# Kernel tuning notes

Measured on AMD Instinct MI355X. Metric: run time of the kernel, lower is better.

The kernel has to match this reference:

```python
import jax, jax.numpy as jnp
import numpy as np

N = 100000   # nodes
E = 3200000  # random edges (before self-loops)
D = 20       # hidden width


def setup_inputs() -> dict:
    key = jax.random.key(0)
    k = jax.random.split(key, 8)
    return {
        "feat": jax.random.normal(k[0], (N, 1), jnp.float32),
        "W_start": jax.random.normal(k[1], (1, D), jnp.float32) * 0.5,
        "b_start": jnp.zeros((D,), jnp.float32),
        "W_mid": jax.random.normal(k[2], (18, D, D), jnp.float32) * (1.0 / np.sqrt(D)),
        "b_mid": jnp.zeros((18, D), jnp.float32),
        "W_final": jax.random.normal(k[3], (D, D), jnp.float32) * (1.0 / np.sqrt(D)),
        "b_final": jnp.zeros((D,), jnp.float32),
        "src": jax.random.randint(k[4], (E,), 0, N, jnp.int32),
        "dst": jax.random.randint(k[5], (E,), 0, N, jnp.int32),
    }


def reference(feat, W_start, b_start, W_mid, b_mid, W_final, b_final, src, dst):
    # dgl.add_self_loop
    loop = jnp.arange(N, dtype=src.dtype)
    src2 = jnp.concatenate([src, loop])
    dst2 = jnp.concatenate([dst, loop])

    ones = jnp.ones(src2.shape[0], jnp.float32)
    out_deg = jax.ops.segment_sum(ones, src2, num_segments=N)
    in_deg = jax.ops.segment_sum(ones, dst2, num_segments=N)
    # with self-loops degrees >= 1; clamp defensively like DGL
    dout = jnp.power(jnp.maximum(out_deg, 1.0), -0.5)  # [N]
    din = jnp.power(jnp.maximum(in_deg, 1.0), -0.5)    # [N]

    def conv(h, W, b):
        # GraphConv norm='both': D_out^{-1/2} on source, sum-aggregate, D_in^{-1/2} on dest
        hw = (h * dout[:, None]) @ W                   # [N, out]
        agg = jax.ops.segment_sum(hw[src2], dst2, num_segments=N)
        return agg * din[:, None] + b

    h = jax.nn.relu(conv(feat, W_start, b_start))

    def step(h, wb):
        W, b = wb
        return jax.nn.relu(conv(h, W, b)), None

    h, _ = jax.lax.scan(step, h, (W_mid, b_mid))
    h = conv(h, W_final, b_final)
    return h[None]  # unsqueeze(0) -> [1, N, D]
```

## Files before the change

kernel.cpp:

```cpp
#include <hip/hip_runtime.h>

#define DH   20
#define BKS  10
#define BKN  1024
#define MAXK 128
#define CHUNK 8192


__global__ void zero_bhist2(int* __restrict__ bhist_d, int* __restrict__ bhist_s) {
    int i = threadIdx.x;
    if (i < MAXK) { bhist_d[i] = 0; bhist_s[i] = 0; }
}

__global__ __launch_bounds__(256) void bucket_hist2(const int* __restrict__ src,
        const int* __restrict__ dst, int* __restrict__ bhist_d,
        int* __restrict__ bhist_s, int E, int K) {
    __shared__ int hd[MAXK];
    __shared__ int hs[MAXK];
    for (int i = threadIdx.x; i < K; i += blockDim.x) { hd[i] = 0; hs[i] = 0; }
    __syncthreads();
    int lo = blockIdx.x * CHUNK;
    int hi = lo + CHUNK; if (hi > E) hi = E;
    for (int e = lo + (int)threadIdx.x; e < hi; e += 256) {
        atomicAdd(&hd[__builtin_nontemporal_load(&dst[e]) >> BKS], 1);
        atomicAdd(&hs[__builtin_nontemporal_load(&src[e]) >> BKS], 1);
    }
    __syncthreads();
    for (int i = threadIdx.x; i < K; i += blockDim.x) {
        if (hd[i]) atomicAdd(&bhist_d[i], hd[i]);
        if (hs[i]) atomicAdd(&bhist_s[i], hs[i]);
    }
}

__global__ void bucket_scan2(const int* __restrict__ bhist_d, int* __restrict__ bbase_d,
                             int* __restrict__ bcursor_d, const int* __restrict__ bhist_s,
                             int* __restrict__ bbase_s, int* __restrict__ bcursor_s, int K) {
    if (threadIdx.x == 0) {
        int run = 0;
        for (int k = 0; k < K; ++k) {
            bbase_d[k] = run; bcursor_d[k] = run;
            run += bhist_d[k];
        }
        bbase_d[K] = run;
    } else if (threadIdx.x == 1) {
        int run = 0;
        for (int k = 0; k < K; ++k) {
            bbase_s[k] = run; bcursor_s[k] = run;
            run += bhist_s[k];
        }
        bbase_s[K] = run;
    }
}

__global__ __launch_bounds__(256) void bucket_place2(const int* __restrict__ src,
        const int* __restrict__ dst, int* __restrict__ bcursor_d,
        int* __restrict__ bcursor_s, int* __restrict__ pairs,
        int* __restrict__ ssort, int E, int K) {
    __shared__ int hd[MAXK];
    __shared__ int hs[MAXK];
    __shared__ int rbd[MAXK];
    __shared__ int rbs[MAXK];
    int lo = blockIdx.x * CHUNK;
    int hi = lo + CHUNK; if (hi > E) hi = E;
    for (int i = threadIdx.x; i < K; i += blockDim.x) { hd[i] = 0; hs[i] = 0; }
    __syncthreads();
    for (int e = lo + (int)threadIdx.x; e < hi; e += 256) {
        atomicAdd(&hd[__builtin_nontemporal_load(&dst[e]) >> BKS], 1);
        atomicAdd(&hs[__builtin_nontemporal_load(&src[e]) >> BKS], 1);
    }
    __syncthreads();
    for (int i = threadIdx.x; i < K; i += blockDim.x) {
        rbd[i] = hd[i] ? atomicAdd(&bcursor_d[i], hd[i]) : 0;
        rbs[i] = hs[i] ? atomicAdd(&bcursor_s[i], hs[i]) : 0;
        hd[i] = 0; hs[i] = 0;
    }
    __syncthreads();
    for (int e = lo + (int)threadIdx.x; e < hi; e += 256) {
        int d = __builtin_nontemporal_load(&dst[e]);
        int s = __builtin_nontemporal_load(&src[e]);
        int bkd = d >> BKS;
        int pd = atomicAdd(&hd[bkd], 1);
        pairs[rbd[bkd] + pd] = (s << BKS) | (d & (BKN - 1));
        int bks = s >> BKS;
        int ps = atomicAdd(&hs[bks], 1);
        ssort[rbs[bks] + ps] = s & (BKN - 1);
    }
}

__global__ __launch_bounds__(256) void bucket_outdeg(const int* __restrict__ bbase_s,
        const int* __restrict__ ssort, double* __restrict__ dout, int n_nodes) {
    __shared__ int h[BKN];
    int k = blockIdx.x;
    int nbase = k << BKS;
    int nrem = n_nodes - nbase; if (nrem > BKN) nrem = BKN;
    for (int i = threadIdx.x; i < BKN; i += 256) h[i] = 1;
    __syncthreads();
    int e0 = bbase_s[k], e1 = bbase_s[k + 1];
    for (int e = e0 + (int)threadIdx.x; e < e1; e += 256)
        atomicAdd(&h[__builtin_nontemporal_load(&ssort[e])], 1);
    __syncthreads();
    for (int i = threadIdx.x; i < nrem; i += 256)
        dout[nbase + i] = 1.0 / sqrt((double)h[i]);
}

__global__ __launch_bounds__(256) void bucket_build(
        const int* __restrict__ bbase, const int* __restrict__ pairs,
        int* __restrict__ row_ptr, double* __restrict__ din,
        int* __restrict__ col, int n_nodes, int n_edges) {
    __shared__ int h[BKN];
    __shared__ int ts[256];
    int k = blockIdx.x;
    int t = threadIdx.x;
    int nbase = k << BKS;
    int nrem = n_nodes - nbase; if (nrem > BKN) nrem = BKN;
    for (int i = t; i < BKN; i += 256) h[i] = 0;
    __syncthreads();
    int e0 = bbase[k], e1 = bbase[k + 1];
    for (int e = e0 + t; e < e1; e += 256)
        atomicAdd(&h[__builtin_nontemporal_load(&pairs[e]) & (BKN - 1)], 1);
    __syncthreads();
    int i0 = t * 4;
    int c0 = h[i0], c1 = h[i0 + 1], c2 = h[i0 + 2], c3 = h[i0 + 3];
    int s = c0 + c1 + c2 + c3;
    ts[t] = s;
    __syncthreads();
    for (int off = 1; off < 256; off <<= 1) {
        int v = (t >= off) ? ts[t - off] : 0;
        __syncthreads();
        ts[t] += v;
        __syncthreads();
    }
    int run = bbase[k] + ts[t] - s;
    int cs[4] = {c0, c1, c2, c3};
#pragma unroll
    for (int j = 0; j < 4; ++j) {
        int idx = i0 + j;
        if (idx < nrem) {
            row_ptr[nbase + idx] = run;
            din[nbase + idx] = 1.0 / sqrt((double)(cs[j] + 1));
        }
        h[idx] = run;
        run += cs[j];
    }
    if (t == 0 && nbase + BKN >= n_nodes) row_ptr[n_nodes] = n_edges;
    __syncthreads();
    for (int e = e0 + t; e < e1; e += 256) {
        int pk = __builtin_nontemporal_load(&pairs[e]);
        int slot = atomicAdd(&h[pk & (BKN - 1)], 1);
        col[slot] = pk >> BKS;
    }
}


__global__ void compute_x0(const float* __restrict__ feat, const double* __restrict__ dout,
                           double* __restrict__ x0, int n) {
    int i = blockIdx.x * blockDim.x + threadIdx.x;
    if (i < n) x0[i] = (double)feat[i] * dout[i];
}

__global__ __launch_bounds__(256) void layer_start(
        const double* __restrict__ x0, const int* __restrict__ row_ptr,
        const int* __restrict__ col, const double* __restrict__ din,
        const double* __restrict__ dout, const float* __restrict__ W,
        const float* __restrict__ b, float* __restrict__ xout, int n_nodes) {
    int n    = (blockIdx.x * blockDim.x + threadIdx.x) >> 6;
    int lane = threadIdx.x & 63;
    if (n >= n_nodes) return;
    double a = (lane == 0) ? x0[n] : 0.0;
    int e0 = row_ptr[n], e1 = row_ptr[n + 1];
    for (int e = e0 + lane; e < e1; e += 64)
        a += x0[__builtin_nontemporal_load(&col[e])];
#pragma unroll
    for (int off = 32; off > 0; off >>= 1)
        a += __shfl_xor(a, off, 64);
    if (lane < DH) {
        double v = a * din[n] * (double)W[lane] + (double)b[lane];
        float r = fmaxf((float)v, 0.0f);
        xout[(long)n * DH + lane] = (float)((double)r * dout[n]);
    }
}

__global__ __launch_bounds__(256) void transform(
        const float* __restrict__ h, const float* __restrict__ W,
        float* __restrict__ y, int n_nodes) {
    __shared__ float Wl[DH * DH];
    for (int i = threadIdx.x; i < DH * DH; i += blockDim.x) Wl[i] = W[i];
    __syncthreads();
    int n = blockIdx.x * blockDim.x + threadIdx.x;
    if (n >= n_nodes) return;
    const float4* h4 = (const float4*)(h + (size_t)n * DH);
    float4 a0 = h4[0], a1 = h4[1], a2 = h4[2], a3 = h4[3], a4 = h4[4];
    float hv[DH] = {a0.x, a0.y, a0.z, a0.w, a1.x, a1.y, a1.z, a1.w,
                    a2.x, a2.y, a2.z, a2.w, a3.x, a3.y, a3.z, a3.w,
                    a4.x, a4.y, a4.z, a4.w};
    double acc[DH];
#pragma unroll
    for (int j = 0; j < DH; ++j) acc[j] = 0.0;
#pragma unroll
    for (int k = 0; k < DH; ++k) {
        double hk = (double)hv[k];
#pragma unroll
        for (int j = 0; j < DH; ++j)
            acc[j] += hk * (double)Wl[k * DH + j];
    }
    float4* y4 = (float4*)(y + (size_t)n * DH);
    y4[0] = make_float4((float)acc[0],  (float)acc[1],  (float)acc[2],  (float)acc[3]);
    y4[1] = make_float4((float)acc[4],  (float)acc[5],  (float)acc[6],  (float)acc[7]);
    y4[2] = make_float4((float)acc[8],  (float)acc[9],  (float)acc[10], (float)acc[11]);
    y4[3] = make_float4((float)acc[12], (float)acc[13], (float)acc[14], (float)acc[15]);
    y4[4] = make_float4((float)acc[16], (float)acc[17], (float)acc[18], (float)acc[19]);
}

__global__ __launch_bounds__(256, 8) void gather_agg(
        const float* __restrict__ y, const int* __restrict__ row_ptr,
        const int* __restrict__ col, const double* __restrict__ din,
        const double* __restrict__ dout, const float* __restrict__ b,
        float* __restrict__ hout, int n_nodes, int mode) {
    int n    = (blockIdx.x * blockDim.x + threadIdx.x) >> 6;
    int lane = threadIdx.x & 63;
    if (n >= n_nodes) return;

    int ep = lane / 5;
    int jq = lane - ep * 5;
    const float4* __restrict__ y4 = (const float4*)y;

    int e0 = row_ptr[n], e1 = row_ptr[n + 1];

    int s0 = -1, s1 = -1, s2 = -1, s3 = -1;
    if (ep < 12) {
        int p = e0 + ep;
        if (p      < e1) s0 = __builtin_nontemporal_load(&col[p]);
        if (p + 12 < e1) s1 = __builtin_nontemporal_load(&col[p + 12]);
        if (p + 24 < e1) s2 = __builtin_nontemporal_load(&col[p + 24]);
        if (p + 36 < e1) s3 = __builtin_nontemporal_load(&col[p + 36]);
    }
    bool p0 = s0 >= 0, p1 = s1 >= 0, p2 = s2 >= 0, p3 = s3 >= 0;
    float4 v0 = y4[(p0 ? s0 : n) * 5 + jq];
    float4 v1 = y4[(p1 ? s1 : n) * 5 + jq];
    float4 v2 = y4[(p2 ? s2 : n) * 5 + jq];
    float4 v3 = y4[(p3 ? s3 : n) * 5 + jq];

    double g[4] = {0.0, 0.0, 0.0, 0.0};
    if (ep == 0) {
        float4 v = y4[n * 5 + jq];
        g[0] = (double)v.x; g[1] = (double)v.y; g[2] = (double)v.z; g[3] = (double)v.w;
    }
    if (p0) { g[0] += (double)v0.x; g[1] += (double)v0.y; g[2] += (double)v0.z; g[3] += (double)v0.w; }
    if (p1) { g[0] += (double)v1.x; g[1] += (double)v1.y; g[2] += (double)v1.z; g[3] += (double)v1.w; }
    if (p2) { g[0] += (double)v2.x; g[1] += (double)v2.y; g[2] += (double)v2.z; g[3] += (double)v2.w; }
    if (p3) { g[0] += (double)v3.x; g[1] += (double)v3.y; g[2] += (double)v3.z; g[3] += (double)v3.w; }

    if (e1 - e0 > 48) {
        if (ep < 12) {
            for (int e = e0 + 48 + ep; e < e1; e += 12) {
                int s = __builtin_nontemporal_load(&col[e]);
                float4 v = y4[s * 5 + jq];
                g[0] += (double)v.x; g[1] += (double)v.y;
                g[2] += (double)v.z; g[3] += (double)v.w;
            }
        }
    }

#define FOLD(LIM, DELTA)                                                        \
    {                                                                           \
        int srcl = lane + DELTA; if (srcl > 63) srcl = lane;                    \
        double t0 = __shfl(g[0], srcl, 64);                                     \
        double t1 = __shfl(g[1], srcl, 64);                                     \
        double t2 = __shfl(g[2], srcl, 64);                                     \
        double t3 = __shfl(g[3], srcl, 64);                                     \
        if (ep < (LIM)) { g[0] += t0; g[1] += t1; g[2] += t2; g[3] += t3; }     \
    }
    FOLD(4, 40)
    FOLD(4, 20)
    FOLD(2, 10)
    FOLD(1, 5)
#undef FOLD

    if (lane < 5) {
        double dn = din[n];
        float4 bb = ((const float4*)b)[lane];
        double o0 = g[0] * dn + (double)bb.x;
        double o1 = g[1] * dn + (double)bb.y;
        double o2 = g[2] * dn + (double)bb.z;
        double o3 = g[3] * dn + (double)bb.w;
        float4 w;
        if (mode == 0) {
            double dd = dout[n];
            w.x = (float)((double)fmaxf((float)o0, 0.0f) * dd);
            w.y = (float)((double)fmaxf((float)o1, 0.0f) * dd);
            w.z = (float)((double)fmaxf((float)o2, 0.0f) * dd);
            w.w = (float)((double)fmaxf((float)o3, 0.0f) * dd);
        } else {
            w.x = (float)o0; w.y = (float)o1; w.z = (float)o2; w.w = (float)o3;
        }
        ((float4*)(hout + (size_t)n * DH))[lane] = w;
    }
}


static inline size_t align256(size_t x) { return (x + 255) & ~(size_t)255; }

extern "C" void kernel_launch(void* const* d_in, const int* in_sizes, int n_in,
                              void* d_out, int out_size, void* d_ws, size_t ws_size,
                              hipStream_t stream) {
    const float* feat    = (const float*)d_in[0];
    const float* W_start = (const float*)d_in[1];
    const float* b_start = (const float*)d_in[2];
    const float* W_mid   = (const float*)d_in[3];
    const float* b_mid   = (const float*)d_in[4];
    const float* W_final = (const float*)d_in[5];
    const float* b_final = (const float*)d_in[6];
    const int*   src     = (const int*)d_in[7];
    const int*   dst     = (const int*)d_in[8];

    const int N = in_sizes[0];
    const int E = in_sizes[7];
    const int L = in_sizes[3] / (DH * DH);
    const int K = (N + BKN - 1) / BKN;

    char* p = (char*)d_ws;
    double* dout_d = (double*)p; p += align256(sizeof(double) * N);
    double* din_d  = (double*)p; p += align256(sizeof(double) * N);
    double* x0     = (double*)p; p += align256(sizeof(double) * N);
    int* row_ptr   = (int*)p;    p += align256(sizeof(int) * (N + 1));
    int* bhist_d   = (int*)p;    p += align256(sizeof(int) * (MAXK + 1));
    int* bbase_d   = (int*)p;    p += align256(sizeof(int) * (MAXK + 1));
    int* bcursor_d = (int*)p;    p += align256(sizeof(int) * (MAXK + 1));
    int* bhist_s   = (int*)p;    p += align256(sizeof(int) * (MAXK + 1));
    int* bbase_s   = (int*)p;    p += align256(sizeof(int) * (MAXK + 1));
    int* bcursor_s = (int*)p;    p += align256(sizeof(int) * (MAXK + 1));
    int* col       = (int*)p;    p += align256(sizeof(int) * E);
    float* hbuf    = (float*)p;  p += align256(sizeof(float) * N * DH);
    float* ybuf    = (float*)p;  p += align256(sizeof(float) * N * DH);
    int* pairs = (int*)hbuf;
    int* ssort = col;

    const int BT = 256;
    int grid_n  = (N + BT - 1) / BT;
    int grid_c  = (E + CHUNK - 1) / CHUNK;
    int grid_nw = (N + 3) / 4;

    zero_bhist2<<<1, MAXK, 0, stream>>>(bhist_d, bhist_s);
    bucket_hist2<<<grid_c, BT, 0, stream>>>(src, dst, bhist_d, bhist_s, E, K);
    bucket_scan2<<<1, 64, 0, stream>>>(bhist_d, bbase_d, bcursor_d,
                                       bhist_s, bbase_s, bcursor_s, K);
    bucket_place2<<<grid_c, BT, 0, stream>>>(src, dst, bcursor_d, bcursor_s,
                                             pairs, ssort, E, K);
    bucket_outdeg<<<K, BT, 0, stream>>>(bbase_s, ssort, dout_d, N);
    bucket_build<<<K, BT, 0, stream>>>(bbase_d, pairs, row_ptr, din_d, col, N, E);

    compute_x0<<<grid_n, BT, 0, stream>>>(feat, dout_d, x0, N);
    layer_start<<<grid_nw, BT, 0, stream>>>(x0, row_ptr, col, din_d, dout_d,
                                            W_start, b_start, hbuf, N);

    for (int l = 0; l < L; ++l) {
        transform<<<grid_n, BT, 0, stream>>>(hbuf, W_mid + (size_t)l * DH * DH, ybuf, N);
        gather_agg<<<grid_nw, BT, 0, stream>>>(ybuf, row_ptr, col, din_d, dout_d,
                                               b_mid + (size_t)l * DH, hbuf, N, 0);
    }

    transform<<<grid_n, BT, 0, stream>>>(hbuf, W_final, ybuf, N);
    gather_agg<<<grid_nw, BT, 0, stream>>>(ybuf, row_ptr, col, din_d, dout_d,
                                           b_final, (float*)d_out, N, 1);
}
```

Before: 1.704 ms.

## Fuse dense transform into gather kernel and shrink CSR-build buckets with LDS staging

Each hidden layer now runs as one kernel. It first aggregates neighbour features and then applies the 20x20 weight through wave shuffles, instead of writing and re-reading an intermediate transformed feature buffer. This relies on the linearity of aggregation and removes one full-array read/write pass and one launch per layer. The CSR build switches to 256-node buckets, which gives more blocks, and uses a parallel shared-memory scan for bucket offsets. It also stages column indices in LDS before a coalesced write-out, at the cost of larger shared-memory use per block.

```diff
diff --git a/kernel.cpp b/kernel.cpp
--- a/kernel.cpp
+++ b/kernel.cpp
@@ -1,9 +1,10 @@
 #include <hip/hip_runtime.h>
 
 #define DH   20
-#define BKS  10
-#define BKN  1024
-#define MAXK 128
+#define BKS  8
+#define BKN  256
+#define MAXK 512
+#define ECAP 10240
 #define CHUNK 8192
 
 
@@ -32,24 +33,30 @@
     }
 }
 
-__global__ void bucket_scan2(const int* __restrict__ bhist_d, int* __restrict__ bbase_d,
-                             int* __restrict__ bcursor_d, const int* __restrict__ bhist_s,
-                             int* __restrict__ bbase_s, int* __restrict__ bcursor_s, int K) {
-    if (threadIdx.x == 0) {
-        int run = 0;
-        for (int k = 0; k < K; ++k) {
-            bbase_d[k] = run; bcursor_d[k] = run;
-            run += bhist_d[k];
-        }
-        bbase_d[K] = run;
-    } else if (threadIdx.x == 1) {
-        int run = 0;
-        for (int k = 0; k < K; ++k) {
-            bbase_s[k] = run; bcursor_s[k] = run;
-            run += bhist_s[k];
-        }
-        bbase_s[K] = run;
-    }
+__global__ __launch_bounds__(512) void bucket_scan2(
+        const int* __restrict__ bhist_d, int* __restrict__ bbase_d,
+        int* __restrict__ bcursor_d, const int* __restrict__ bhist_s,
+        int* __restrict__ bbase_s, int* __restrict__ bcursor_s, int K) {
+    __shared__ int a[512];
+    __shared__ int b[512];
+    int t = threadIdx.x;
+    int vd = (t < K) ? bhist_d[t] : 0;
+    int vs = (t < K) ? bhist_s[t] : 0;
+    a[t] = vd; b[t] = vs;
+    __syncthreads();
+    for (int off = 1; off < 512; off <<= 1) {
+        int x = (t >= off) ? a[t - off] : 0;
+        int y = (t >= off) ? b[t - off] : 0;
+        __syncthreads();
+        a[t] += x; b[t] += y;
+        __syncthreads();
+    }
+    if (t < K) {
+        int ed = a[t] - vd, es = b[t] - vs;
+        bbase_d[t] = ed; bcursor_d[t] = ed;
+        bbase_s[t] = es; bcursor_s[t] = es;
+    }
+    if (t == K - 1) { bbase_d[K] = a[t]; bbase_s[K] = b[t]; }
 }
 
 __global__ __launch_bounds__(256) void bucket_place2(const int* __restrict__ src,
@@ -91,16 +98,16 @@
         const int* __restrict__ ssort, double* __restrict__ dout, int n_nodes) {
     __shared__ int h[BKN];
     int k = blockIdx.x;
+    int t = threadIdx.x;
     int nbase = k << BKS;
     int nrem = n_nodes - nbase; if (nrem > BKN) nrem = BKN;
-    for (int i = threadIdx.x; i < BKN; i += 256) h[i] = 1;
+    h[t] = 1;
     __syncthreads();
     int e0 = bbase_s[k], e1 = bbase_s[k + 1];
-    for (int e = e0 + (int)threadIdx.x; e < e1; e += 256)
+    for (int e = e0 + t; e < e1; e += 256)
         atomicAdd(&h[__builtin_nontemporal_load(&ssort[e])], 1);
     __syncthreads();
-    for (int i = threadIdx.x; i < nrem; i += 256)
-        dout[nbase + i] = 1.0 / sqrt((double)h[i]);
+    if (t < nrem) dout[nbase + t] = 1.0 / sqrt((double)h[t]);
 }
 
 __global__ __launch_bounds__(256) void bucket_build(
@@ -108,21 +115,20 @@
         int* __restrict__ row_ptr, double* __restrict__ din,
         int* __restrict__ col, int n_nodes, int n_edges) {
     __shared__ int h[BKN];
-    __shared__ int ts[256];
+    __shared__ int ts[BKN];
+    __shared__ int ecol[ECAP];
     int k = blockIdx.x;
     int t = threadIdx.x;
     int nbase = k << BKS;
     int nrem = n_nodes - nbase; if (nrem > BKN) nrem = BKN;
-    for (int i = t; i < BKN; i += 256) h[i] = 0;
+    h[t] = 0;
     __syncthreads();
     int e0 = bbase[k], e1 = bbase[k + 1];
     for (int e = e0 + t; e < e1; e += 256)
         atomicAdd(&h[__builtin_nontemporal_load(&pairs[e]) & (BKN - 1)], 1);
     __syncthreads();
-    int i0 = t * 4;
-    int c0 = h[i0], c1 = h[i0 + 1], c2 = h[i0 + 2], c3 = h[i0 + 3];
-    int s = c0 + c1 + c2 + c3;
-    ts[t] = s;
+    int c = h[t];
+    ts[t] = c;
     __syncthreads();
     for (int off = 1; off < 256; off <<= 1) {
         int v = (t >= off) ? ts[t - off] : 0;
@@ -130,25 +136,25 @@
         ts[t] += v;
         __syncthreads();
     }
-    int run = bbase[k] + ts[t] - s;
-    int cs[4] = {c0, c1, c2, c3};
-#pragma unroll
-    for (int j = 0; j < 4; ++j) {
-        int idx = i0 + j;
-        if (idx < nrem) {
-            row_ptr[nbase + idx] = run;
-            din[nbase + idx] = 1.0 / sqrt((double)(cs[j] + 1));
-        }
-        h[idx] = run;
-        run += cs[j];
-    }
+    int run = ts[t] - c;
+    if (t < nrem) {
+        row_ptr[nbase + t] = e0 + run;
+        din[nbase + t] = 1.0 / sqrt((double)(c + 1));
+    }
+    h[t] = run;
     if (t == 0 && nbase + BKN >= n_nodes) row_ptr[n_nodes] = n_edges;
     __syncthreads();
+    int cnt = e1 - e0;
     for (int e = e0 + t; e < e1; e += 256) {
         int pk = __builtin_nontemporal_load(&pairs[e]);
         int slot = atomicAdd(&h[pk & (BKN - 1)], 1);
-        col[slot] = pk >> BKS;
-    }
+        if (slot < ECAP) ecol[slot] = pk >> BKS;
+        else col[e0 + slot] = pk >> BKS;
+    }
+    __syncthreads();
+    int lim = cnt < ECAP ? cnt : ECAP;
+    for (int i = t; i < lim; i += 256)
+        col[e0 + i] = ecol[i];
 }
 
 
@@ -180,49 +186,23 @@
     }
 }
 
-__global__ __launch_bounds__(256) void transform(
-        const float* __restrict__ h, const float* __restrict__ W,
-        float* __restrict__ y, int n_nodes) {
+__global__ __launch_bounds__(256, 8) void layer_fused(
+        const float* __restrict__ x, const int* __restrict__ row_ptr,
+        const int* __restrict__ col, const double* __restrict__ din,
+        const double* __restrict__ dout, const float* __restrict__ W,
+        const float* __restrict__ b, float* __restrict__ xout,
+        int n_nodes, int mode) {
     __shared__ float Wl[DH * DH];
     for (int i = threadIdx.x; i < DH * DH; i += blockDim.x) Wl[i] = W[i];
     __syncthreads();
-    int n = blockIdx.x * blockDim.x + threadIdx.x;
-    if (n >= n_nodes) return;
-    const float4* h4 = (const float4*)(h + (size_t)n * DH);
-    float4 a0 = h4[0], a1 = h4[1], a2 = h4[2], a3 = h4[3], a4 = h4[4];
-    float hv[DH] = {a0.x, a0.y, a0.z, a0.w, a1.x, a1.y, a1.z, a1.w,
-                    a2.x, a2.y, a2.z, a2.w, a3.x, a3.y, a3.z, a3.w,
-                    a4.x, a4.y, a4.z, a4.w};
-    double acc[DH];
-#pragma unroll
-    for (int j = 0; j < DH; ++j) acc[j] = 0.0;
-#pragma unroll
-    for (int k = 0; k < DH; ++k) {
-        double hk = (double)hv[k];
-#pragma unroll
-        for (int j = 0; j < DH; ++j)
-            acc[j] += hk * (double)Wl[k * DH + j];
-    }
-    float4* y4 = (float4*)(y + (size_t)n * DH);
-    y4[0] = make_float4((float)acc[0],  (float)acc[1],  (float)acc[2],  (float)acc[3]);
-    y4[1] = make_float4((float)acc[4],  (float)acc[5],  (float)acc[6],  (float)acc[7]);
-    y4[2] = make_float4((float)acc[8],  (float)acc[9],  (float)acc[10], (float)acc[11]);
-    y4[3] = make_float4((float)acc[12], (float)acc[13], (float)acc[14], (float)acc[15]);
-    y4[4] = make_float4((float)acc[16], (float)acc[17], (float)acc[18], (float)acc[19]);
-}
-
-__global__ __launch_bounds__(256, 8) void gather_agg(
-        const float* __restrict__ y, const int* __restrict__ row_ptr,
-        const int* __restrict__ col, const double* __restrict__ din,
-        const double* __restrict__ dout, const float* __restrict__ b,
-        float* __restrict__ hout, int n_nodes, int mode) {
+
     int n    = (blockIdx.x * blockDim.x + threadIdx.x) >> 6;
     int lane = threadIdx.x & 63;
     if (n >= n_nodes) return;
 
     int ep = lane / 5;
     int jq = lane - ep * 5;
-    const float4* __restrict__ y4 = (const float4*)y;
+    const float4* __restrict__ x4 = (const float4*)x;
 
     int e0 = row_ptr[n], e1 = row_ptr[n + 1];
 
@@ -235,14 +215,14 @@
         if (p + 36 < e1) s3 = __builtin_nontemporal_load(&col[p + 36]);
     }
     bool p0 = s0 >= 0, p1 = s1 >= 0, p2 = s2 >= 0, p3 = s3 >= 0;
-    float4 v0 = y4[(p0 ? s0 : n) * 5 + jq];
-    float4 v1 = y4[(p1 ? s1 : n) * 5 + jq];
-    float4 v2 = y4[(p2 ? s2 : n) * 5 + jq];
-    float4 v3 = y4[(p3 ? s3 : n) * 5 + jq];
+    float4 v0 = x4[(p0 ? s0 : n) * 5 + jq];
+    float4 v1 = x4[(p1 ? s1 : n) * 5 + jq];
+    float4 v2 = x4[(p2 ? s2 : n) * 5 + jq];
+    float4 v3 = x4[(p3 ? s3 : n) * 5 + jq];
 
     double g[4] = {0.0, 0.0, 0.0, 0.0};
     if (ep == 0) {
-        float4 v = y4[n * 5 + jq];
+        float4 v = x4[n * 5 + jq];
         g[0] = (double)v.x; g[1] = (double)v.y; g[2] = (double)v.z; g[3] = (double)v.w;
     }
     if (p0) { g[0] += (double)v0.x; g[1] += (double)v0.y; g[2] += (double)v0.z; g[3] += (double)v0.w; }
@@ -254,7 +234,7 @@
         if (ep < 12) {
             for (int e = e0 + 48 + ep; e < e1; e += 12) {
                 int s = __builtin_nontemporal_load(&col[e]);
-                float4 v = y4[s * 5 + jq];
+                float4 v = x4[s * 5 + jq];
                 g[0] += (double)v.x; g[1] += (double)v.y;
                 g[2] += (double)v.z; g[3] += (double)v.w;
             }
@@ -276,24 +256,22 @@
     FOLD(1, 5)
 #undef FOLD
 
-    if (lane < 5) {
-        double dn = din[n];
-        float4 bb = ((const float4*)b)[lane];
-        double o0 = g[0] * dn + (double)bb.x;
-        double o1 = g[1] * dn + (double)bb.y;
-        double o2 = g[2] * dn + (double)bb.z;
-        double o3 = g[3] * dn + (double)bb.w;
-        float4 w;
+    int jj = (lane < DH) ? lane : 0;
+    double acc = 0.0;
+#pragma unroll
+    for (int k = 0; k < DH; ++k) {
+        double gk = __shfl(g[k & 3], k >> 2, 64);
+        acc += gk * (double)Wl[k * DH + jj];
+    }
+
+    if (lane < DH) {
+        double v = acc * din[n] + (double)b[lane];
         if (mode == 0) {
-            double dd = dout[n];
-            w.x = (float)((double)fmaxf((float)o0, 0.0f) * dd);
-            w.y = (float)((double)fmaxf((float)o1, 0.0f) * dd);
-            w.z = (float)((double)fmaxf((float)o2, 0.0f) * dd);
-            w.w = (float)((double)fmaxf((float)o3, 0.0f) * dd);
+            float r = fmaxf((float)v, 0.0f);
+            xout[(long)n * DH + lane] = (float)((double)r * dout[n]);
         } else {
-            w.x = (float)o0; w.y = (float)o1; w.z = (float)o2; w.w = (float)o3;
+            xout[(long)n * DH + lane] = (float)v;
         }
-        ((float4*)(hout + (size_t)n * DH))[lane] = w;
     }
 }
 
@@ -330,9 +308,9 @@
     int* bbase_s   = (int*)p;    p += align256(sizeof(int) * (MAXK + 1));
     int* bcursor_s = (int*)p;    p += align256(sizeof(int) * (MAXK + 1));
     int* col       = (int*)p;    p += align256(sizeof(int) * E);
-    float* hbuf    = (float*)p;  p += align256(sizeof(float) * N * DH);
-    float* ybuf    = (float*)p;  p += align256(sizeof(float) * N * DH);
-    int* pairs = (int*)hbuf;
+    float* xa      = (float*)p;  p += align256(sizeof(float) * N * DH);
+    float* xb      = (float*)p;  p += align256(sizeof(float) * N * DH);
+    int* pairs = (int*)xa;
     int* ssort = col;
 
     const int BT = 256;
@@ -342,8 +320,8 @@
 
     zero_bhist2<<<1, MAXK, 0, stream>>>(bhist_d, bhist_s);
     bucket_hist2<<<grid_c, BT, 0, stream>>>(src, dst, bhist_d, bhist_s, E, K);
-    bucket_scan2<<<1, 64, 0, stream>>>(bhist_d, bbase_d, bcursor_d,
-                                       bhist_s, bbase_s, bcursor_s, K);
+    bucket_scan2<<<1, 512, 0, stream>>>(bhist_d, bbase_d, bcursor_d,
+                                        bhist_s, bbase_s, bcursor_s, K);
     bucket_place2<<<grid_c, BT, 0, stream>>>(src, dst, bcursor_d, bcursor_s,
                                              pairs, ssort, E, K);
     bucket_outdeg<<<K, BT, 0, stream>>>(bbase_s, ssort, dout_d, N);
@@ -351,15 +329,17 @@
 
     compute_x0<<<grid_n, BT, 0, stream>>>(feat, dout_d, x0, N);
     layer_start<<<grid_nw, BT, 0, stream>>>(x0, row_ptr, col, din_d, dout_d,
-                                            W_start, b_start, hbuf, N);
-
+                                            W_start, b_start, xa, N);
+
+    float* xin = xa;
+    float* xot = xb;
     for (int l = 0; l < L; ++l) {
-        transform<<<grid_n, BT, 0, stream>>>(hbuf, W_mid + (size_t)l * DH * DH, ybuf, N);
-        gather_agg<<<grid_nw, BT, 0, stream>>>(ybuf, row_ptr, col, din_d, dout_d,
-                                               b_mid + (size_t)l * DH, hbuf, N, 0);
-    }
-
-    transform<<<grid_n, BT, 0, stream>>>(hbuf, W_final, ybuf, N);
-    gather_agg<<<grid_nw, BT, 0, stream>>>(ybuf, row_ptr, col, din_d, dout_d,
-                                           b_final, (float*)d_out, N, 1);
-}
+        layer_fused<<<grid_nw, BT, 0, stream>>>(xin, row_ptr, col, din_d, dout_d,
+                                                W_mid + (size_t)l * DH * DH,
+                                                b_mid + (size_t)l * DH, xot, N, 0);
+        float* t = xin; xin = xot; xot = t;
+    }
+
+    layer_fused<<<grid_nw, BT, 0, stream>>>(xin, row_ptr, col, din_d, dout_d,
+                                            W_final, b_final, (float*)d_out, N, 1);
+}
```

New measurement: 2.139 ms. 25.5% more time.

## Split CSR build into finer 256-node buckets with LDS-staged column writes

Applied to the files above, without the earlier changes.

The CSR build kernel now uses four blocks per coarse 1024-node bucket. Each block scans the whole coarse bucket, keeps only its own 256-node sub-range, and finds its base offset by counting earlier edges with a reduction. Column indices are staged in LDS and written out contiguously, and a block-to-XCD remap is added. The single-thread serial bucket scan is replaced by a parallel shared-memory scan. This raises parallelism (about 98 to about 391 blocks) and coalesces the col writes, at the cost of each pairs entry being read four times.

```diff
diff --git a/kernel.cpp b/kernel.cpp
--- a/kernel.cpp
+++ b/kernel.cpp
@@ -1,29 +1,32 @@
 #include <hip/hip_runtime.h>
 
-#define DH   20
-#define BKS  10
-#define BKN  1024
-#define MAXK 128
+#define DH    20
+#define BKSC  10
+#define BKC   1024
+#define MAXKC 128
+#define BKSF  8
+#define BKF   256
+#define ECAP  10240
 #define CHUNK 8192
 
 
 __global__ void zero_bhist2(int* __restrict__ bhist_d, int* __restrict__ bhist_s) {
     int i = threadIdx.x;
-    if (i < MAXK) { bhist_d[i] = 0; bhist_s[i] = 0; }
+    if (i < MAXKC) { bhist_d[i] = 0; bhist_s[i] = 0; }
 }
 
 __global__ __launch_bounds__(256) void bucket_hist2(const int* __restrict__ src,
         const int* __restrict__ dst, int* __restrict__ bhist_d,
         int* __restrict__ bhist_s, int E, int K) {
-    __shared__ int hd[MAXK];
-    __shared__ int hs[MAXK];
+    __shared__ int hd[MAXKC];
+    __shared__ int hs[MAXKC];
     for (int i = threadIdx.x; i < K; i += blockDim.x) { hd[i] = 0; hs[i] = 0; }
     __syncthreads();
     int lo = blockIdx.x * CHUNK;
     int hi = lo + CHUNK; if (hi > E) hi = E;
     for (int e = lo + (int)threadIdx.x; e < hi; e += 256) {
-        atomicAdd(&hd[__builtin_nontemporal_load(&dst[e]) >> BKS], 1);
-        atomicAdd(&hs[__builtin_nontemporal_load(&src[e]) >> BKS], 1);
+        atomicAdd(&hd[__builtin_nontemporal_load(&dst[e]) >> BKSC], 1);
+        atomicAdd(&hs[__builtin_nontemporal_load(&src[e]) >> BKSC], 1);
     }
     __syncthreads();
     for (int i = threadIdx.x; i < K; i += blockDim.x) {
@@ -32,41 +35,47 @@
     }
 }
 
-__global__ void bucket_scan2(const int* __restrict__ bhist_d, int* __restrict__ bbase_d,
-                             int* __restrict__ bcursor_d, const int* __restrict__ bhist_s,
-                             int* __restrict__ bbase_s, int* __restrict__ bcursor_s, int K) {
-    if (threadIdx.x == 0) {
-        int run = 0;
-        for (int k = 0; k < K; ++k) {
-            bbase_d[k] = run; bcursor_d[k] = run;
-            run += bhist_d[k];
-        }
-        bbase_d[K] = run;
-    } else if (threadIdx.x == 1) {
-        int run = 0;
-        for (int k = 0; k < K; ++k) {
-            bbase_s[k] = run; bcursor_s[k] = run;
-            run += bhist_s[k];
-        }
-        bbase_s[K] = run;
-    }
+__global__ __launch_bounds__(128) void bucket_scan2(
+        const int* __restrict__ bhist_d, int* __restrict__ bbase_d,
+        int* __restrict__ bcursor_d, const int* __restrict__ bhist_s,
+        int* __restrict__ bbase_s, int* __restrict__ bcursor_s, int K) {
+    __shared__ int a[MAXKC];
+    __shared__ int b[MAXKC];
+    int t = threadIdx.x;
+    int vd = (t < K) ? bhist_d[t] : 0;
+    int vs = (t < K) ? bhist_s[t] : 0;
+    a[t] = vd; b[t] = vs;
+    __syncthreads();
+    for (int off = 1; off < 128; off <<= 1) {
+        int x = (t >= off) ? a[t - off] : 0;
+        int y = (t >= off) ? b[t - off] : 0;
+        __syncthreads();
+        a[t] += x; b[t] += y;
+        __syncthreads();
+    }
+    if (t < K) {
+        int ed = a[t] - vd, es = b[t] - vs;
+        bbase_d[t] = ed; bcursor_d[t] = ed;
+        bbase_s[t] = es; bcursor_s[t] = es;
+    }
+    if (t == K - 1) { bbase_d[K] = a[t]; bbase_s[K] = b[t]; }
 }
 
 __global__ __launch_bounds__(256) void bucket_place2(const int* __restrict__ src,
         const int* __restrict__ dst, int* __restrict__ bcursor_d,
         int* __restrict__ bcursor_s, int* __restrict__ pairs,
         int* __restrict__ ssort, int E, int K) {
-    __shared__ int hd[MAXK];
-    __shared__ int hs[MAXK];
-    __shared__ int rbd[MAXK];
-    __shared__ int rbs[MAXK];
+    __shared__ int hd[MAXKC];
+    __shared__ int hs[MAXKC];
+    __shared__ int rbd[MAXKC];
+    __shared__ int rbs[MAXKC];
     int lo = blockIdx.x * CHUNK;
     int hi = lo + CHUNK; if (hi > E) hi = E;
     for (int i = threadIdx.x; i < K; i += blockDim.x) { hd[i] = 0; hs[i] = 0; }
     __syncthreads();
     for (int e = lo + (int)threadIdx.x; e < hi; e += 256) {
-        atomicAdd(&hd[__builtin_nontemporal_load(&dst[e]) >> BKS], 1);
-        atomicAdd(&hs[__builtin_nontemporal_load(&src[e]) >> BKS], 1);
+        atomicAdd(&hd[__builtin_nontemporal_load(&dst[e]) >> BKSC], 1);
+        atomicAdd(&hs[__builtin_nontemporal_load(&src[e]) >> BKSC], 1);
     }
     __syncthreads();
     for (int i = threadIdx.x; i < K; i += blockDim.x) {
@@ -78,28 +87,29 @@
     for (int e = lo + (int)threadIdx.x; e < hi; e += 256) {
         int d = __builtin_nontemporal_load(&dst[e]);
         int s = __builtin_nontemporal_load(&src[e]);
-        int bkd = d >> BKS;
+        int bkd = d >> BKSC;
         int pd = atomicAdd(&hd[bkd], 1);
-        pairs[rbd[bkd] + pd] = (s << BKS) | (d & (BKN - 1));
-        int bks = s >> BKS;
+        pairs[rbd[bkd] + pd] = (s << BKSC) | (d & (BKC - 1));
+        int bks = s >> BKSC;
         int ps = atomicAdd(&hs[bks], 1);
-        ssort[rbs[bks] + ps] = s & (BKN - 1);
+        ssort[rbs[bks] + ps] = s & (BKC - 1);
     }
 }
 
 __global__ __launch_bounds__(256) void bucket_outdeg(const int* __restrict__ bbase_s,
         const int* __restrict__ ssort, double* __restrict__ dout, int n_nodes) {
-    __shared__ int h[BKN];
+    __shared__ int h[BKC];
     int k = blockIdx.x;
-    int nbase = k << BKS;
-    int nrem = n_nodes - nbase; if (nrem > BKN) nrem = BKN;
-    for (int i = threadIdx.x; i < BKN; i += 256) h[i] = 1;
+    int t = threadIdx.x;
+    int nbase = k << BKSC;
+    int nrem = n_nodes - nbase; if (nrem > BKC) nrem = BKC;
+    for (int i = t; i < BKC; i += 256) h[i] = 1;
     __syncthreads();
     int e0 = bbase_s[k], e1 = bbase_s[k + 1];
-    for (int e = e0 + (int)threadIdx.x; e < e1; e += 256)
+    for (int e = e0 + t; e < e1; e += 256)
         atomicAdd(&h[__builtin_nontemporal_load(&ssort[e])], 1);
     __syncthreads();
-    for (int i = threadIdx.x; i < nrem; i += 256)
+    for (int i = t; i < nrem; i += 256)
         dout[nbase + i] = 1.0 / sqrt((double)h[i]);
 }
 
@@ -107,22 +117,40 @@
         const int* __restrict__ bbase, const int* __restrict__ pairs,
         int* __restrict__ row_ptr, double* __restrict__ din,
         int* __restrict__ col, int n_nodes, int n_edges) {
-    __shared__ int h[BKN];
-    __shared__ int ts[256];
-    int k = blockIdx.x;
+    __shared__ int h[BKF];
+    __shared__ int ts[BKF];
+    __shared__ int red[256];
+    __shared__ int ecol[ECAP];
+    int nwg = gridDim.x;
+    int xcd = blockIdx.x & 7;
+    int loc = blockIdx.x >> 3;
+    int q = nwg >> 3, r = nwg & 7;
+    int k = ((xcd < r) ? xcd * (q + 1) : r * (q + 1) + (xcd - r) * q) + loc;
+    int kc = k >> 2;
+    int f  = k & 3;
     int t = threadIdx.x;
-    int nbase = k << BKS;
-    int nrem = n_nodes - nbase; if (nrem > BKN) nrem = BKN;
-    for (int i = t; i < BKN; i += 256) h[i] = 0;
-    __syncthreads();
-    int e0 = bbase[k], e1 = bbase[k + 1];
-    for (int e = e0 + t; e < e1; e += 256)
-        atomicAdd(&h[__builtin_nontemporal_load(&pairs[e]) & (BKN - 1)], 1);
-    __syncthreads();
-    int i0 = t * 4;
-    int c0 = h[i0], c1 = h[i0 + 1], c2 = h[i0 + 2], c3 = h[i0 + 3];
-    int s = c0 + c1 + c2 + c3;
-    ts[t] = s;
+    int nbase = k << BKSF;
+    int nrem = n_nodes - nbase; if (nrem > BKF) nrem = BKF;
+    h[t] = 0;
+    __syncthreads();
+    int e0 = bbase[kc], e1 = bbase[kc + 1];
+    int before = 0;
+    for (int e = e0 + t; e < e1; e += 256) {
+        int pk = pairs[e];
+        int dl = pk & (BKC - 1);
+        int fe = dl >> BKSF;
+        if (fe == f) atomicAdd(&h[dl & (BKF - 1)], 1);
+        else if (fe < f) ++before;
+    }
+    red[t] = before;
+    __syncthreads();
+    for (int off = 128; off > 0; off >>= 1) {
+        if (t < off) red[t] += red[t + off];
+        __syncthreads();
+    }
+    int fbase = e0 + red[0];
+    int c = h[t];
+    ts[t] = c;
     __syncthreads();
     for (int off = 1; off < 256; off <<= 1) {
         int v = (t >= off) ? ts[t - off] : 0;
@@ -130,25 +158,28 @@
         ts[t] += v;
         __syncthreads();
     }
-    int run = bbase[k] + ts[t] - s;
-    int cs[4] = {c0, c1, c2, c3};
-#pragma unroll
-    for (int j = 0; j < 4; ++j) {
-        int idx = i0 + j;
-        if (idx < nrem) {
-            row_ptr[nbase + idx] = run;
-            din[nbase + idx] = 1.0 / sqrt((double)(cs[j] + 1));
+    int lx = ts[t] - c;
+    if (t < nrem) {
+        row_ptr[nbase + t] = fbase + lx;
+        din[nbase + t] = 1.0 / sqrt((double)(c + 1));
+    }
+    h[t] = lx;
+    if (t == 0 && nbase + BKF >= n_nodes) row_ptr[n_nodes] = n_edges;
+    __syncthreads();
+    for (int e = e0 + t; e < e1; e += 256) {
+        int pk = pairs[e];
+        int dl = pk & (BKC - 1);
+        if ((dl >> BKSF) == f) {
+            int slot = atomicAdd(&h[dl & (BKF - 1)], 1);
+            if (slot < ECAP) ecol[slot] = pk >> BKSC;
+            else col[fbase + slot] = pk >> BKSC;
         }
-        h[idx] = run;
-        run += cs[j];
-    }
-    if (t == 0 && nbase + BKN >= n_nodes) row_ptr[n_nodes] = n_edges;
-    __syncthreads();
-    for (int e = e0 + t; e < e1; e += 256) {
-        int pk = __builtin_nontemporal_load(&pairs[e]);
-        int slot = atomicAdd(&h[pk & (BKN - 1)], 1);
-        col[slot] = pk >> BKS;
-    }
+    }
+    __syncthreads();
+    int cnt = ts[BKF - 1];
+    int lim = cnt < ECAP ? cnt : ECAP;
+    for (int i = t; i < lim; i += 256)
+        col[fbase + i] = ecol[i];
 }
 
 
@@ -316,19 +347,20 @@
     const int N = in_sizes[0];
     const int E = in_sizes[7];
     const int L = in_sizes[3] / (DH * DH);
-    const int K = (N + BKN - 1) / BKN;
+    const int KC = (N + BKC - 1) / BKC;
+    const int KF = (N + BKF - 1) / BKF;
 
     char* p = (char*)d_ws;
     double* dout_d = (double*)p; p += align256(sizeof(double) * N);
     double* din_d  = (double*)p; p += align256(sizeof(double) * N);
     double* x0     = (double*)p; p += align256(sizeof(double) * N);
     int* row_ptr   = (int*)p;    p += align256(sizeof(int) * (N + 1));
-    int* bhist_d   = (int*)p;    p += align256(sizeof(int) * (MAXK + 1));
-    int* bbase_d   = (int*)p;    p += align256(sizeof(int) * (MAXK + 1));
-    int* bcursor_d = (int*)p;    p += align256(sizeof(int) * (MAXK + 1));
-    int* bhist_s   = (int*)p;    p += align256(sizeof(int) * (MAXK + 1));
-    int* bbase_s   = (int*)p;    p += align256(sizeof(int) * (MAXK + 1));
-    int* bcursor_s = (int*)p;    p += align256(sizeof(int) * (MAXK + 1));
+    int* bhist_d   = (int*)p;    p += align256(sizeof(int) * (MAXKC + 1));
+    int* bbase_d   = (int*)p;    p += align256(sizeof(int) * (MAXKC + 1));
+    int* bcursor_d = (int*)p;    p += align256(sizeof(int) * (MAXKC + 1));
+    int* bhist_s   = (int*)p;    p += align256(sizeof(int) * (MAXKC + 1));
+    int* bbase_s   = (int*)p;    p += align256(sizeof(int) * (MAXKC + 1));
+    int* bcursor_s = (int*)p;    p += align256(sizeof(int) * (MAXKC + 1));
     int* col       = (int*)p;    p += align256(sizeof(int) * E);
     float* hbuf    = (float*)p;  p += align256(sizeof(float) * N * DH);
     float* ybuf    = (float*)p;  p += align256(sizeof(float) * N * DH);
@@ -340,14 +372,14 @@
     int grid_c  = (E + CHUNK - 1) / CHUNK;
     int grid_nw = (N + 3) / 4;
 
-    zero_bhist2<<<1, MAXK, 0, stream>>>(bhist_d, bhist_s);
-    bucket_hist2<<<grid_c, BT, 0, stream>>>(src, dst, bhist_d, bhist_s, E, K);
-    bucket_scan2<<<1, 64, 0, stream>>>(bhist_d, bbase_d, bcursor_d,
-                                       bhist_s, bbase_s, bcursor_s, K);
+    zero_bhist2<<<1, MAXKC, 0, stream>>>(bhist_d, bhist_s);
+    bucket_hist2<<<grid_c, BT, 0, stream>>>(src, dst, bhist_d, bhist_s, E, KC);
+    bucket_scan2<<<1, 128, 0, stream>>>(bhist_d, bbase_d, bcursor_d,
+                                        bhist_s, bbase_s, bcursor_s, KC);
     bucket_place2<<<grid_c, BT, 0, stream>>>(src, dst, bcursor_d, bcursor_s,
-                                             pairs, ssort, E, K);
-    bucket_outdeg<<<K, BT, 0, stream>>>(bbase_s, ssort, dout_d, N);
-    bucket_build<<<K, BT, 0, stream>>>(bbase_d, pairs, row_ptr, din_d, col, N, E);
+                                             pairs, ssort, E, KC);
+    bucket_outdeg<<<KC, BT, 0, stream>>>(bbase_s, ssort, dout_d, N);
+    bucket_build<<<KF, BT, 0, stream>>>(bbase_d, pairs, row_ptr, din_d, col, N, E);
 
     compute_x0<<<grid_n, BT, 0, stream>>>(feat, dout_d, x0, N);
     layer_start<<<grid_nw, BT, 0, stream>>>(x0, row_ptr, col, din_d, dout_d,
```

Result: faster. 1.660 ms (-2.6%).
